# Kernel tuning notes

Measured on AMD Instinct MI355X. Metric: run time of the kernel, lower is better.

## Reference

```python
import jax, jax.numpy as jnp
import numpy as np

B, N, C, K1, K2, TD = 4, 4096, 128, 16, 8, 64
CIN = 2 * (3 + C)  # 262


def setup_inputs() -> dict:
    key = jax.random.key(0)
    ks = jax.random.split(key, 8)
    s = 0.05
    feature = jax.random.normal(ks[0], (B, C, N), jnp.float32)
    xyz = jax.random.normal(ks[1], (B, 3, N), jnp.float32)
    wq = jax.random.normal(ks[2], (TD, CIN), jnp.float32) * s
    wk = jax.random.normal(ks[3], (TD, CIN), jnp.float32) * s
    wv = jax.random.normal(ks[4], (TD, CIN), jnp.float32) * s
    w1 = jax.random.normal(ks[5], (C, TD), jnp.float32) * s
    bq = jnp.zeros((TD,), jnp.float32)
    bk = jnp.zeros((TD,), jnp.float32)
    bv = jnp.zeros((TD,), jnp.float32)
    b1 = jnp.zeros((C,), jnp.float32)
    return {"feature": feature, "xyz": xyz, "wq": wq, "bq": bq,
            "wk": wk, "bk": bk, "wv": wv, "bv": bv, "w1": w1, "b1": b1}


def _group(x, ind):
    # x: [B, Cx, N], ind: [B, N, K] -> [B, Cx, K, N]; g[b,c,k,n] = x[b,c,ind[b,n,k]]
    g = jnp.take_along_axis(x[:, :, None, :], ind[:, None, :, :], axis=3)  # [B,Cx,N,K]
    return g.transpose(0, 1, 3, 2)


def reference(feature, xyz, wq, bq, wk, bk, wv, bv, w1, b1):
    # --- KNN (self-included then dropped), idx[b,n,k] = k-th nearest of point n ---
    sq = jnp.sum(xyz * xyz, axis=1)                                   # [B,N]
    dist = sq[:, :, None] + sq[:, None, :] - 2.0 * jnp.einsum('bdn,bdm->bnm', xyz, xyz)
    _, idx = jax.lax.top_k(-dist, K1 + 1)                             # [B,N,17]
    idx = idx[:, :, 1:]                                               # drop self -> [B,N,16]
    idx1 = idx[:, :, :K2]                                             # [B,N,8]

    gxyz = _group(xyz, idx)        # [B,3,16,N]
    gxyz1 = _group(xyz, idx1)      # [B,3,8,N]
    gfea = _group(feature, idx)    # [B,C,16,N]
    gfea1 = _group(feature, idx1)  # [B,C,8,N]

    rel_xyz = gxyz - xyz[:, :, None, :]
    rel_xyz1 = gxyz1 - xyz[:, :, None, :]
    rel_fea = gfea - feature[:, :, None, :]
    rel_fea1 = gfea1 - feature[:, :, None, :]

    def relpos(rx, rf, K):
        return jnp.concatenate([
            rx,
            jnp.broadcast_to(xyz[:, :, None, :], (B, 3, K, N)),
            rf,
            jnp.broadcast_to(feature[:, :, None, :], (B, C, K, N)),
        ], axis=1)  # [B,262,K,N]

    rel_pos = relpos(rel_xyz, rel_fea, K1)     # [B,262,16,N]
    rel_pos1 = relpos(rel_xyz1, rel_fea1, K2)  # [B,262,8,N]

    # 1x1 Conv2d projections
    q = jnp.einsum('oc,bckn->bokn', wq, rel_pos1) + bq[None, :, None, None]  # [B,64,8,N]
    k = jnp.einsum('oc,bckn->bokn', wk, rel_pos) + bk[None, :, None, None]   # [B,64,16,N]
    v = jnp.einsum('oc,bckn->bokn', wv, rel_pos) + bv[None, :, None, None]   # [B,64,16,N]

    attn = jnp.einsum('bmnf,bmjf->bnjf', q, k)   # [B,8,16,N]
    attn = jax.nn.softmax(attn, axis=-2)         # softmax over j (16 neighbors)
    res = jnp.einsum('bnjf,bmjf->bmf', attn, v)  # [B,64,N]

    out = jnp.einsum('om,bmf->bof', w1, res) + b1[None, :, None]  # Conv1d 64->128
    return out + feature
```

## Files before the change

kernel.cpp:

```cpp
#include <hip/hip_runtime.h>

#define NN 4096
#define CCH 128

__global__ __launch_bounds__(256) void transpose_w(
    const float* __restrict__ wq, const float* __restrict__ wk, const float* __restrict__ wv,
    const float* __restrict__ w1, const float* __restrict__ xyz,
    float* __restrict__ wTq, float* __restrict__ wTk, float* __restrict__ wTv,
    float* __restrict__ w1T, float* __restrict__ wPack, float4* __restrict__ pts4) {
  int t = blockIdx.x * 256 + threadIdx.x;
  if (t < 64 * 262) {
    int o = t / 262, c = t - o * 262;
    wTq[c * 64 + o] = wq[t];
    wTk[c * 64 + o] = wk[t];
    wTv[c * 64 + o] = wv[t];
  }
  if (t < 128 * 64) {
    int r = t >> 6, c2 = t & 63;
    w1T[c2 * 128 + r] = w1[t];
  }
  if (t < 49152) {
    int r = t & 3, o = (t >> 2) & 63;
    int g = t >> 8;
    int ct = g / 6, mh = g - ct * 6;
    int m = mh >> 1, h = mh & 1;
    const float* wsrc = (m == 0) ? wq : ((m == 1) ? wk : wv);
    wPack[t] = wsrc[o * 262 + (h ? 134 : 6) + 4 * ct + r];
  }
  if (t < 4 * NN) {
    int bb = t >> 12, i = t & 4095;
    const float* xb = xyz + (size_t)bb * 3 * NN;
    float x = xb[i], y = xb[NN + i], z = xb[2 * NN + i];
    pts4[t] = make_float4(x, y, z, x * x + y * y + z * z);
  }
}

__global__ __launch_bounds__(1024, 4) void knn_half(const float4* __restrict__ pts4,
                                                    unsigned long long* __restrict__ keys_ws) {
  __shared__ float bufA[64 * 64];
  __shared__ float bufB[64 * 64];
  __shared__ unsigned long long hits[32 * 65];
  __shared__ int cnt[64];
  const int b  = blockIdx.x >> 7;
  const int g  = (blockIdx.x >> 1) & 63;
  const int h  = blockIdx.x & 1;
  const int n0 = g << 6;
  const int ql = threadIdx.x & 63;
  const int ch = __builtin_amdgcn_readfirstlane(threadIdx.x >> 6);
  if (threadIdx.x < 64) cnt[threadIdx.x] = 0;
  const int q = n0 + ql;
  const float4* pb4 = pts4 + ((size_t)b << 12);
  const float4 me = pb4[q];
  float bd0 = 3.0e38f, bd1 = 3.0e38f, bd2 = 3.0e38f, bd3 = 3.0e38f;
  const int m0 = (h << 11) + (ch << 7);
  for (int mb = m0; mb < m0 + 128; mb += 8) {
    float4 P[8];
#pragma unroll
    for (int u = 0; u < 8; ++u) P[u] = pb4[mb + u];
#pragma unroll
    for (int u = 0; u < 8; ++u) {
      float d = me.w + P[u].w - 2.0f * (me.x * P[u].x + me.y * P[u].y + me.z * P[u].z);
      d = (mb + u == q) ? 3.0e38f : d;
      bd3 = __builtin_amdgcn_fmed3f(d, bd2, bd3);
      bd2 = __builtin_amdgcn_fmed3f(d, bd1, bd2);
      bd1 = __builtin_amdgcn_fmed3f(d, bd0, bd1);
      bd0 = fminf(bd0, d);
    }
  }
  {
    const int r0 = (ch * 4) * 64 + ql;
    bufA[r0] = bd0; bufA[r0 + 64] = bd1; bufA[r0 + 128] = bd2; bufA[r0 + 192] = bd3;
  }
  __syncthreads();
  if (ch < 8) {
    const int a0 = (2 * ch) * 4, b0 = (2 * ch + 1) * 4;
    float o8[8]; int pa = 0, pb = 0;
#pragma unroll
    for (int k = 0; k < 8; ++k) {
      float va = (pa < 4) ? bufA[(a0 + pa) * 64 + ql] : 3.0e38f;
      float vb = (pb < 4) ? bufA[(b0 + pb) * 64 + ql] : 3.0e38f;
      bool ta = va <= vb;
      o8[k] = ta ? va : vb;
      pa += ta ? 1 : 0; pb += ta ? 0 : 1;
    }
#pragma unroll
    for (int k = 0; k < 8; ++k) bufB[(ch * 8 + k) * 64 + ql] = o8[k];
  }
  __syncthreads();
  if (ch < 4) {
    const int a0 = (2 * ch) * 8, b0 = (2 * ch + 1) * 8;
    float o16[16]; int pa = 0, pb = 0;
#pragma unroll
    for (int k = 0; k < 16; ++k) {
      float va = (pa < 8) ? bufB[(a0 + pa) * 64 + ql] : 3.0e38f;
      float vb = (pb < 8) ? bufB[(b0 + pb) * 64 + ql] : 3.0e38f;
      bool ta = va <= vb;
      o16[k] = ta ? va : vb;
      pa += ta ? 1 : 0; pb += ta ? 0 : 1;
    }
#pragma unroll
    for (int k = 0; k < 16; ++k) bufA[(ch * 16 + k) * 64 + ql] = o16[k];
  }
  __syncthreads();
  if (ch < 2) {
    const int a0 = (2 * ch) * 16, b0 = (2 * ch + 1) * 16;
    float o16[16]; int pa = 0, pb = 0;
#pragma unroll
    for (int k = 0; k < 16; ++k) {
      float va = bufA[(a0 + pa) * 64 + ql];
      float vb = bufA[(b0 + pb) * 64 + ql];
      bool ta = va <= vb;
      o16[k] = ta ? va : vb;
      pa += ta ? 1 : 0; pb += ta ? 0 : 1;
    }
#pragma unroll
    for (int k = 0; k < 16; ++k) bufB[(ch * 16 + k) * 64 + ql] = o16[k];
  }
  __syncthreads();
  if (ch == 0) {
    float v = 0.f; int pa = 0, pb = 0;
#pragma unroll
    for (int k = 0; k < 16; ++k) {
      float va = bufB[pa * 64 + ql];
      float vb = bufB[(16 + pb) * 64 + ql];
      bool ta = va <= vb;
      v = ta ? va : vb;
      pa += ta ? 1 : 0; pb += ta ? 0 : 1;
    }
    bufA[15 * 64 + ql] = v;
  }
  __syncthreads();
  const float tau = bufA[15 * 64 + ql];
  for (int mb = m0; mb < m0 + 128; mb += 8) {
    float4 P[8];
#pragma unroll
    for (int u = 0; u < 8; ++u) P[u] = pb4[mb + u];
#pragma unroll
    for (int u = 0; u < 8; ++u) {
      float d = me.w + P[u].w - 2.0f * (me.x * P[u].x + me.y * P[u].y + me.z * P[u].z);
      if (d <= tau && (mb + u) != q) {
        int pos = atomicAdd(&cnt[ql], 1);
        if (pos < 32) {
          unsigned int f = __float_as_uint(d);
          f ^= (f >> 31) ? 0xFFFFFFFFu : 0x80000000u;
          hits[pos * 65 + ql] = ((unsigned long long)f << 32) | (unsigned int)(mb + u);
        }
      }
    }
  }
  __syncthreads();
  const int l5 = threadIdx.x & 31;
#pragma unroll
  for (int t = 0; t < 2; ++t) {
    const int qq = (t * 1024 + (int)threadIdx.x) >> 5;
    int nv = cnt[qq]; nv = nv > 32 ? 32 : nv;
    unsigned long long key = (l5 < nv) ? hits[l5 * 65 + qq] : ~0ULL;
#pragma unroll
    for (int k = 2; k <= 32; k <<= 1) {
#pragma unroll
      for (int jm = k >> 1; jm > 0; jm >>= 1) {
        unsigned long long o2 = __shfl_xor(key, jm, 32);
        bool asc = ((l5 & k) == 0);
        bool lower = ((l5 & jm) == 0);
        unsigned long long mn = key < o2 ? key : o2;
        unsigned long long mx = key < o2 ? o2 : key;
        key = (lower == asc) ? mn : mx;
      }
    }
    if (l5 < 16) {
      const size_t gq = (size_t)((b << 12) + n0 + qq);
      keys_ws[((size_t)h << 18) + gq * 16 + l5] = key;
    }
  }
}

__global__ __launch_bounds__(256) void knn_merge(const unsigned long long* __restrict__ keys_ws,
                                                 int* __restrict__ idxout) {
  const int gq = blockIdx.x * 256 + threadIdx.x;
  const unsigned long long* A  = keys_ws + (size_t)gq * 16;
  const unsigned long long* Bp = keys_ws + (1u << 18) + (size_t)gq * 16;
  int* op = idxout + (size_t)gq * 16;
  int pa = 0, pb = 0;
#pragma unroll
  for (int k = 0; k < 16; ++k) {
    unsigned long long va = A[pa], vb = Bp[pb];
    bool ta = va <= vb;
    op[k] = (int)((ta ? va : vb) & 0xFFFFFFFFu);
    pa += ta ? 1 : 0; pb += ta ? 0 : 1;
  }
}

__global__ __launch_bounds__(512) void proj_kernel(
    const float* __restrict__ feature, const float* __restrict__ xyz,
    const float* __restrict__ wTq, const float* __restrict__ wTk, const float* __restrict__ wTv,
    const float* __restrict__ wPack,
    const float* __restrict__ bq, const float* __restrict__ bk, const float* __restrict__ bv,
    float* __restrict__ uqA, float* __restrict__ cq,
    float2* __restrict__ ukv,
    float* __restrict__ ck, float* __restrict__ cv) {
  __shared__ float fl[64][132];
  __shared__ float4 wl[16 * 6 * 64];
  const int p0 = blockIdx.x << 6;
  const int b  = p0 >> 12;
  const int n0 = p0 & 4095;
  {
    const int i  = threadIdx.x & 63;
    const int c0 = threadIdx.x >> 6;
    const float* fb = feature + (size_t)b * CCH * NN + n0 + i;
    for (int cc = c0; cc < CCH; cc += 8) fl[i][cc] = fb[(size_t)cc * NN];
    if (threadIdx.x < 192) {
      const int d = threadIdx.x >> 6;
      fl[i][128 + d] = xyz[((size_t)b * 3 + d) * NN + n0 + i];
    }
  }
  const int o  = threadIdx.x & 63;
  const int pg = threadIdx.x >> 6;
  const float4* wp = reinterpret_cast<const float4*>(wPack);
  float aU[3][8], aT[3][8];
#pragma unroll
  for (int mm = 0; mm < 3; ++mm)
#pragma unroll
    for (int s = 0; s < 8; ++s) { aU[mm][s] = 0.f; aT[mm][s] = 0.f; }

  for (int half = 0; half < 2; ++half) {
    __syncthreads();
    for (int d4 = threadIdx.x; d4 < 6144; d4 += 512)
      wl[d4] = wp[half * 6144 + d4];
    __syncthreads();
#pragma unroll 4
    for (int ct = 0; ct < 16; ++ct) {
      float4 w4[6];
#pragma unroll
      for (int mh = 0; mh < 6; ++mh) w4[mh] = wl[(ct * 6 + mh) * 64 + o];
      const int cglob = half * 16 + ct;
#pragma unroll
      for (int s = 0; s < 8; ++s) {
        const float4 f4 = *reinterpret_cast<const float4*>(&fl[pg * 8 + s][4 * cglob]);
#pragma unroll
        for (int mm = 0; mm < 3; ++mm) {
          aU[mm][s] += w4[2 * mm].x * f4.x + w4[2 * mm].y * f4.y + w4[2 * mm].z * f4.z + w4[2 * mm].w * f4.w;
          aT[mm][s] += w4[2 * mm + 1].x * f4.x + w4[2 * mm + 1].y * f4.y + w4[2 * mm + 1].z * f4.z + w4[2 * mm + 1].w * f4.w;
        }
      }
    }
  }
  float wxu[3][3], wxt[3][3];
#pragma unroll
  for (int dd = 0; dd < 3; ++dd) {
    wxu[0][dd] = wTq[dd * 64 + o]; wxt[0][dd] = wTq[(3 + dd) * 64 + o];
    wxu[1][dd] = wTk[dd * 64 + o]; wxt[1][dd] = wTk[(3 + dd) * 64 + o];
    wxu[2][dd] = wTv[dd * 64 + o]; wxt[2][dd] = wTv[(3 + dd) * 64 + o];
  }
  const float bo0 = bq[o], bo1 = bk[o], bo2 = bv[o];
#pragma unroll
  for (int s = 0; s < 8; ++s) {
    const int p = pg * 8 + s;
    const float x = fl[p][128], y = fl[p][129], z = fl[p][130];
    const size_t gp = ((size_t)(p0 + p)) * 64 + o;
    float uu, tt;
    uu = aU[0][s] + wxu[0][0] * x + wxu[0][1] * y + wxu[0][2] * z;
    tt = aT[0][s] + wxt[0][0] * x + wxt[0][1] * y + wxt[0][2] * z;
    uqA[gp] = uu; cq[gp] = tt + bo0 - uu;
    const float uk_ = aU[1][s] + wxu[1][0] * x + wxu[1][1] * y + wxu[1][2] * z;
    tt = aT[1][s] + wxt[1][0] * x + wxt[1][1] * y + wxt[1][2] * z;
    ck[gp] = tt + bo1 - uk_;
    const float uv_ = aU[2][s] + wxu[2][0] * x + wxu[2][1] * y + wxu[2][2] * z;
    tt = aT[2][s] + wxt[2][0] * x + wxt[2][1] * y + wxt[2][2] * z;
    cv[gp] = tt + bo2 - uv_;
    ukv[gp] = make_float2(uk_, uv_);
  }
}

__global__ __launch_bounds__(256) void attn_core(
    const int* __restrict__ idx,
    const float* __restrict__ uqA, const float* __restrict__ cq,
    const float2* __restrict__ ukv,
    const float* __restrict__ ck, const float* __restrict__ cv,
    float* __restrict__ res_ws) {
  __shared__ float kq[4][24][68];
  const int slot = threadIdx.x >> 6;
  const int o    = threadIdx.x & 63;
  const int p = (blockIdx.x << 2) + slot;
  const int b = p >> 12;
  const int myidx = idx[(size_t)p * 16 + (o & 15)];
  const size_t pb = (size_t)p * 64 + o;
  const float cqo = cq[pb], cko = ck[pb], cvo = cv[pb];
  const int rowbase = (b << 12) * 64;
  float v[16];
#pragma unroll
  for (int j = 0; j < 16; ++j) {
    int nb = __shfl(myidx, j);
    int row = rowbase + nb * 64 + o;
    float2 kv = ukv[row];
    kq[slot][j][o] = kv.x + cko;
    v[j] = kv.y + cvo;
    if (j < 8) kq[slot][16 + j][o] = uqA[row] + cqo;
  }
  const int i  = o >> 3;
  const int jj = o & 7;
  const float* qrow = &kq[slot][16 + i][0];
  const float* k0r  = &kq[slot][jj][0];
  const float* k1r  = &kq[slot][8 + jj][0];
  float s0 = 0.f, s1 = 0.f;
#pragma unroll
  for (int t = 0; t < 16; ++t) {
    float4 q4 = *reinterpret_cast<const float4*>(qrow + 4 * t);
    float4 a4 = *reinterpret_cast<const float4*>(k0r + 4 * t);
    float4 c4 = *reinterpret_cast<const float4*>(k1r + 4 * t);
    s0 += q4.x * a4.x + q4.y * a4.y + q4.z * a4.z + q4.w * a4.w;
    s1 += q4.x * c4.x + q4.y * c4.y + q4.z * c4.z + q4.w * c4.w;
  }
  float mx = fmaxf(s0, s1);
  mx = fmaxf(mx, __shfl_xor(mx, 1));
  mx = fmaxf(mx, __shfl_xor(mx, 2));
  mx = fmaxf(mx, __shfl_xor(mx, 4));
  float e0 = __expf(s0 - mx), e1 = __expf(s1 - mx);
  float den = e0 + e1;
  den += __shfl_xor(den, 1);
  den += __shfl_xor(den, 2);
  den += __shfl_xor(den, 4);
  const float inv = 1.0f / den;
  float w0 = e0 * inv, w1s = e1 * inv;
  w0 += __shfl_xor(w0, 8);   w1s += __shfl_xor(w1s, 8);
  w0 += __shfl_xor(w0, 16);  w1s += __shfl_xor(w1s, 16);
  w0 += __shfl_xor(w0, 32);  w1s += __shfl_xor(w1s, 32);
  float res = 0.f;
#pragma unroll
  for (int j = 0; j < 8; ++j) {
    res += __shfl(w0, j)  * v[j];
    res += __shfl(w1s, j) * v[j + 8];
  }
  res_ws[pb] = res;
}

__global__ __launch_bounds__(512) void out_kernel(
    const float* __restrict__ feature, const float* __restrict__ res,
    const float* __restrict__ w1T, const float* __restrict__ b1,
    float* __restrict__ out) {
  __shared__ float rT[64][66];
  const int p0 = blockIdx.x << 6;
  const int b  = p0 >> 12;
  const int n0 = p0 & 4095;
  {
    const int o = threadIdx.x & 63;
    for (int pp = threadIdx.x >> 6; pp < 64; pp += 8)
      rT[o][pp] = res[(size_t)(p0 + pp) * 64 + o];
  }
  __syncthreads();
  const int n = threadIdx.x & 63;
  const int c0 = (threadIdx.x >> 6) * 16;
  float acc[16];
#pragma unroll
  for (int cc = 0; cc < 16; ++cc) acc[cc] = b1[c0 + cc];
  for (int o = 0; o < 64; ++o) {
    const float rr = rT[o][n];
    const float* wrow = &w1T[o * 128 + c0];
#pragma unroll
    for (int cc = 0; cc < 16; ++cc) acc[cc] += wrow[cc] * rr;
  }
#pragma unroll
  for (int cc = 0; cc < 16; ++cc) {
    const size_t gi = ((size_t)(b * 128 + c0 + cc) << 12) + n0 + n;
    out[gi] = acc[cc] + feature[gi];
  }
}

extern "C" void kernel_launch(void* const* d_in, const int* in_sizes, int n_in,
                              void* d_out, int out_size, void* d_ws, size_t ws_size,
                              hipStream_t stream) {
  const float* feature = (const float*)d_in[0];
  const float* xyz     = (const float*)d_in[1];
  const float* wq      = (const float*)d_in[2];
  const float* bq      = (const float*)d_in[3];
  const float* wk      = (const float*)d_in[4];
  const float* bk      = (const float*)d_in[5];
  const float* wv      = (const float*)d_in[6];
  const float* bv      = (const float*)d_in[7];
  const float* w1      = (const float*)d_in[8];
  const float* b1      = (const float*)d_in[9];
  float* out = (float*)d_out;

  char* ws = (char*)d_ws;
  int*    idx  = (int*)ws;
  float4* pts4 = (float4*)(ws + (1u << 20));
  float*  uqA  = (float*)(ws + (2u << 20));
  float*  cq   = (float*)(ws + (6u << 20));
  float*  ck   = (float*)(ws + (10u << 20));
  float*  cv   = (float*)(ws + (14u << 20));
  float2* ukv  = (float2*)(ws + (18u << 20));
  float*  res  = (float*)(ws + (26u << 20));
  float*  wTq  = (float*)(ws + (30u << 20));
  float*  wTk  = wTq + 262 * 64;
  float*  wTv  = wTk + 262 * 64;
  float*  w1T  = wTv + 262 * 64;
  float*  wPk  = w1T + 128 * 64;
  unsigned long long* keys = (unsigned long long*)(ws + (2u << 20));

  transpose_w<<<192, 256, 0, stream>>>(wq, wk, wv, w1, xyz, wTq, wTk, wTv, w1T, wPk, pts4);
  knn_half<<<512, 1024, 0, stream>>>(pts4, keys);
  knn_merge<<<64, 256, 0, stream>>>(keys, idx);
  proj_kernel<<<256, 512, 0, stream>>>(feature, xyz, wTq, wTk, wTv, wPk, bq, bk, bv,
                                       uqA, cq, ukv, ck, cv);
  attn_core<<<4096, 256, 0, stream>>>(idx, uqA, cq, ukv, ck, cv, res);
  out_kernel<<<256, 512, 0, stream>>>(feature, res, w1T, b1, out);
}
```

Measured before the change: 218.3 us.

## Fuse KNN and projection into one launch with block-range dispatch

Merges the independent knn_half and proj_kernel into a single kernel. The first 256 blocks compute the projections and the remaining 512 blocks do the KNN half-scans, so both run concurrently and one launch plus one serialization point is removed. The projection path is retuned for 1024 threads with 4 points per thread, and weights are read straight from global memory instead of being staged in LDS. The keys workspace moves so it no longer aliases the uqA buffer that the projection now writes concurrently. The shared-memory union and launch_bounds(1024,8) may force register limits that hurt the KNN path.

```diff
diff --git a/kernel.cpp b/kernel.cpp
--- a/kernel.cpp
+++ b/kernel.cpp
@@ -35,15 +35,93 @@
   }
 }
 
-__global__ __launch_bounds__(1024, 4) void knn_half(const float4* __restrict__ pts4,
-                                                    unsigned long long* __restrict__ keys_ws) {
-  __shared__ float bufA[64 * 64];
-  __shared__ float bufB[64 * 64];
-  __shared__ unsigned long long hits[32 * 65];
-  __shared__ int cnt[64];
-  const int b  = blockIdx.x >> 7;
-  const int g  = (blockIdx.x >> 1) & 63;
-  const int h  = blockIdx.x & 1;
+__global__ __launch_bounds__(1024, 8) void fused_knn_proj(
+    const float4* __restrict__ pts4, unsigned long long* __restrict__ keys_ws,
+    const float* __restrict__ feature, const float* __restrict__ xyz,
+    const float* __restrict__ wTq, const float* __restrict__ wTk, const float* __restrict__ wTv,
+    const float* __restrict__ wPack,
+    const float* __restrict__ bq, const float* __restrict__ bk, const float* __restrict__ bv,
+    float* __restrict__ uqA, float* __restrict__ cq,
+    float2* __restrict__ ukv,
+    float* __restrict__ ck, float* __restrict__ cv) {
+  __shared__ __align__(16) char smem[49664];
+
+  if (blockIdx.x < 256) {
+    float (*fl)[132] = (float (*)[132])smem;
+    const int p0 = blockIdx.x << 6;
+    const int b  = p0 >> 12;
+    const int n0 = p0 & 4095;
+    {
+      const int i  = threadIdx.x & 63;
+      const int c0 = threadIdx.x >> 6;
+      const float* fb = feature + (size_t)b * CCH * NN + n0 + i;
+      for (int cc = c0; cc < CCH; cc += 16) fl[i][cc] = fb[(size_t)cc * NN];
+      if (threadIdx.x < 192) {
+        const int d = threadIdx.x >> 6;
+        fl[i][128 + d] = xyz[((size_t)b * 3 + d) * NN + n0 + i];
+      }
+    }
+    __syncthreads();
+    const int o  = threadIdx.x & 63;
+    const int pg = threadIdx.x >> 6;
+    const float4* wp = reinterpret_cast<const float4*>(wPack);
+    float aU[3][4], aT[3][4];
+#pragma unroll
+    for (int mm = 0; mm < 3; ++mm)
+#pragma unroll
+      for (int s = 0; s < 4; ++s) { aU[mm][s] = 0.f; aT[mm][s] = 0.f; }
+    for (int ct = 0; ct < 32; ++ct) {
+      float4 f4[4];
+#pragma unroll
+      for (int s = 0; s < 4; ++s)
+        f4[s] = *reinterpret_cast<const float4*>(&fl[pg * 4 + s][4 * ct]);
+#pragma unroll
+      for (int mm = 0; mm < 3; ++mm) {
+        const float4 wu = wp[(ct * 6 + 2 * mm) * 64 + o];
+        const float4 wt = wp[(ct * 6 + 2 * mm + 1) * 64 + o];
+#pragma unroll
+        for (int s = 0; s < 4; ++s) {
+          aU[mm][s] += wu.x * f4[s].x + wu.y * f4[s].y + wu.z * f4[s].z + wu.w * f4[s].w;
+          aT[mm][s] += wt.x * f4[s].x + wt.y * f4[s].y + wt.z * f4[s].z + wt.w * f4[s].w;
+        }
+      }
+    }
+    float wxu[3][3], wxt[3][3];
+#pragma unroll
+    for (int dd = 0; dd < 3; ++dd) {
+      wxu[0][dd] = wTq[dd * 64 + o]; wxt[0][dd] = wTq[(3 + dd) * 64 + o];
+      wxu[1][dd] = wTk[dd * 64 + o]; wxt[1][dd] = wTk[(3 + dd) * 64 + o];
+      wxu[2][dd] = wTv[dd * 64 + o]; wxt[2][dd] = wTv[(3 + dd) * 64 + o];
+    }
+    const float bo0 = bq[o], bo1 = bk[o], bo2 = bv[o];
+#pragma unroll
+    for (int s = 0; s < 4; ++s) {
+      const int p = pg * 4 + s;
+      const float x = fl[p][128], y = fl[p][129], z = fl[p][130];
+      const size_t gp = ((size_t)(p0 + p)) * 64 + o;
+      float uu, tt;
+      uu = aU[0][s] + wxu[0][0] * x + wxu[0][1] * y + wxu[0][2] * z;
+      tt = aT[0][s] + wxt[0][0] * x + wxt[0][1] * y + wxt[0][2] * z;
+      uqA[gp] = uu; cq[gp] = tt + bo0 - uu;
+      const float uk_ = aU[1][s] + wxu[1][0] * x + wxu[1][1] * y + wxu[1][2] * z;
+      tt = aT[1][s] + wxt[1][0] * x + wxt[1][1] * y + wxt[1][2] * z;
+      ck[gp] = tt + bo1 - uk_;
+      const float uv_ = aU[2][s] + wxu[2][0] * x + wxu[2][1] * y + wxu[2][2] * z;
+      tt = aT[2][s] + wxt[2][0] * x + wxt[2][1] * y + wxt[2][2] * z;
+      cv[gp] = tt + bo2 - uv_;
+      ukv[gp] = make_float2(uk_, uv_);
+    }
+    return;
+  }
+
+  float* bufA = (float*)smem;
+  float* bufB = (float*)(smem + 16384);
+  unsigned long long* hits = (unsigned long long*)(smem + 32768);
+  int* cnt = (int*)(smem + 49408);
+  const int kb = blockIdx.x - 256;
+  const int b  = kb >> 7;
+  const int g  = (kb >> 1) & 63;
+  const int h  = kb & 1;
   const int n0 = g << 6;
   const int ql = threadIdx.x & 63;
   const int ch = __builtin_amdgcn_readfirstlane(threadIdx.x >> 6);
@@ -187,87 +265,6 @@
     bool ta = va <= vb;
     op[k] = (int)((ta ? va : vb) & 0xFFFFFFFFu);
     pa += ta ? 1 : 0; pb += ta ? 0 : 1;
-  }
-}
-
-__global__ __launch_bounds__(512) void proj_kernel(
-    const float* __restrict__ feature, const float* __restrict__ xyz,
-    const float* __restrict__ wTq, const float* __restrict__ wTk, const float* __restrict__ wTv,
-    const float* __restrict__ wPack,
-    const float* __restrict__ bq, const float* __restrict__ bk, const float* __restrict__ bv,
-    float* __restrict__ uqA, float* __restrict__ cq,
-    float2* __restrict__ ukv,
-    float* __restrict__ ck, float* __restrict__ cv) {
-  __shared__ float fl[64][132];
-  __shared__ float4 wl[16 * 6 * 64];
-  const int p0 = blockIdx.x << 6;
-  const int b  = p0 >> 12;
-  const int n0 = p0 & 4095;
-  {
-    const int i  = threadIdx.x & 63;
-    const int c0 = threadIdx.x >> 6;
-    const float* fb = feature + (size_t)b * CCH * NN + n0 + i;
-    for (int cc = c0; cc < CCH; cc += 8) fl[i][cc] = fb[(size_t)cc * NN];
-    if (threadIdx.x < 192) {
-      const int d = threadIdx.x >> 6;
-      fl[i][128 + d] = xyz[((size_t)b * 3 + d) * NN + n0 + i];
-    }
-  }
-  const int o  = threadIdx.x & 63;
-  const int pg = threadIdx.x >> 6;
-  const float4* wp = reinterpret_cast<const float4*>(wPack);
-  float aU[3][8], aT[3][8];
-#pragma unroll
-  for (int mm = 0; mm < 3; ++mm)
-#pragma unroll
-    for (int s = 0; s < 8; ++s) { aU[mm][s] = 0.f; aT[mm][s] = 0.f; }
-
-  for (int half = 0; half < 2; ++half) {
-    __syncthreads();
-    for (int d4 = threadIdx.x; d4 < 6144; d4 += 512)
-      wl[d4] = wp[half * 6144 + d4];
-    __syncthreads();
-#pragma unroll 4
-    for (int ct = 0; ct < 16; ++ct) {
-      float4 w4[6];
-#pragma unroll
-      for (int mh = 0; mh < 6; ++mh) w4[mh] = wl[(ct * 6 + mh) * 64 + o];
-      const int cglob = half * 16 + ct;
-#pragma unroll
-      for (int s = 0; s < 8; ++s) {
-        const float4 f4 = *reinterpret_cast<const float4*>(&fl[pg * 8 + s][4 * cglob]);
-#pragma unroll
-        for (int mm = 0; mm < 3; ++mm) {
-          aU[mm][s] += w4[2 * mm].x * f4.x + w4[2 * mm].y * f4.y + w4[2 * mm].z * f4.z + w4[2 * mm].w * f4.w;
-          aT[mm][s] += w4[2 * mm + 1].x * f4.x + w4[2 * mm + 1].y * f4.y + w4[2 * mm + 1].z * f4.z + w4[2 * mm + 1].w * f4.w;
-        }
-      }
-    }
-  }
-  float wxu[3][3], wxt[3][3];
-#pragma unroll
-  for (int dd = 0; dd < 3; ++dd) {
-    wxu[0][dd] = wTq[dd * 64 + o]; wxt[0][dd] = wTq[(3 + dd) * 64 + o];
-    wxu[1][dd] = wTk[dd * 64 + o]; wxt[1][dd] = wTk[(3 + dd) * 64 + o];
-    wxu[2][dd] = wTv[dd * 64 + o]; wxt[2][dd] = wTv[(3 + dd) * 64 + o];
-  }
-  const float bo0 = bq[o], bo1 = bk[o], bo2 = bv[o];
-#pragma unroll
-  for (int s = 0; s < 8; ++s) {
-    const int p = pg * 8 + s;
-    const float x = fl[p][128], y = fl[p][129], z = fl[p][130];
-    const size_t gp = ((size_t)(p0 + p)) * 64 + o;
-    float uu, tt;
-    uu = aU[0][s] + wxu[0][0] * x + wxu[0][1] * y + wxu[0][2] * z;
-    tt = aT[0][s] + wxt[0][0] * x + wxt[0][1] * y + wxt[0][2] * z;
-    uqA[gp] = uu; cq[gp] = tt + bo0 - uu;
-    const float uk_ = aU[1][s] + wxu[1][0] * x + wxu[1][1] * y + wxu[1][2] * z;
-    tt = aT[1][s] + wxt[1][0] * x + wxt[1][1] * y + wxt[1][2] * z;
-    ck[gp] = tt + bo1 - uk_;
-    const float uv_ = aU[2][s] + wxu[2][0] * x + wxu[2][1] * y + wxu[2][2] * z;
-    tt = aT[2][s] + wxt[2][0] * x + wxt[2][1] * y + wxt[2][2] * z;
-    cv[gp] = tt + bo2 - uv_;
-    ukv[gp] = make_float2(uk_, uv_);
   }
 }
 
@@ -394,13 +391,12 @@
   float*  wTv  = wTk + 262 * 64;
   float*  w1T  = wTv + 262 * 64;
   float*  wPk  = w1T + 128 * 64;
-  unsigned long long* keys = (unsigned long long*)(ws + (2u << 20));
+  unsigned long long* keys = (unsigned long long*)(ws + (31u << 20));
 
   transpose_w<<<192, 256, 0, stream>>>(wq, wk, wv, w1, xyz, wTq, wTk, wTv, w1T, wPk, pts4);
-  knn_half<<<512, 1024, 0, stream>>>(pts4, keys);
+  fused_knn_proj<<<768, 1024, 0, stream>>>(pts4, keys, feature, xyz, wTq, wTk, wTv, wPk,
+                                           bq, bk, bv, uqA, cq, ukv, ck, cv);
   knn_merge<<<64, 256, 0, stream>>>(keys, idx);
-  proj_kernel<<<256, 512, 0, stream>>>(feature, xyz, wTq, wTk, wTv, wPk, bq, bk, bv,
-                                       uqA, cq, ukv, ck, cv);
   attn_core<<<4096, 256, 0, stream>>>(idx, uqA, cq, ukv, ck, cv, res);
   out_kernel<<<256, 512, 0, stream>>>(feature, res, w1T, b1, out);
 }
```

Measured after the change: 253.1 us. 15.9% more time.
